# Kernel tuning notes

Hardware: AMD Instinct MI355X
Metric: run time of the kernel (lower is better)

The kernel has to match this reference:

```python
import jax, jax.numpy as jnp
import numpy as np
import math


def _alibi_slopes(h):
    # h must be a power of 2 here (h=16); matches pow2slopes in the source
    start = 2.0 ** (-2.0 ** (-(math.log2(h) - 3.0)))
    return jnp.asarray([start ** (i + 1) for i in range(h)], dtype=jnp.float32)


def setup_inputs() -> dict:
    key = jax.random.key(0)
    ks = jax.random.split(key, 7)
    B, N, d, h, r = 2, 2048, 1024, 16, 32
    dk = d // h
    x = jax.random.normal(ks[0], (B, N, d), dtype=jnp.float32)
    # causal additive mask (standard usage of the optional `mask` arg)
    i = jnp.arange(N)[:, None]
    j = jnp.arange(N)[None, :]
    mask = jnp.where(j > i, jnp.float32(-1e9), jnp.float32(0.0))[None, None]  # [1,1,N,N]
    s = 1.0 / math.sqrt(d)
    Wq = jax.random.normal(ks[1], (d, d), dtype=jnp.float32) * s
    Wk = jax.random.normal(ks[2], (d, d), dtype=jnp.float32) * s
    Wv = jax.random.normal(ks[3], (d, d), dtype=jnp.float32) * s
    # orthogonal init of U, as in nn.init.orthogonal_
    U, _ = jnp.linalg.qr(jax.random.normal(ks[4], (dk, r), dtype=jnp.float32))
    Wproj = jax.random.normal(ks[5], (d, h * r), dtype=jnp.float32) * (1.0 / math.sqrt(h * r))
    return {"x": x, "mask": mask, "Wq": Wq, "Wk": Wk, "Wv": Wv, "U": U,
            "Wproj": Wproj, "rel_bias_tokens": N}


def reference(x, mask, Wq, Wk, Wv, U, Wproj, rel_bias_tokens):
    B, N, d = x.shape
    dk, r = U.shape
    h = d // dk

    def lowrank_proj(W):
        # Linear(d,d,bias=False) then per-head low-rank projection by U
        y = (x @ W.T).reshape(B, N, h, dk)          # [B,N,h,dk]
        return jnp.einsum('bnhk,kr->bhnr', y, U)     # [B,h,N,r]

    q = lowrank_proj(Wq)
    k = lowrank_proj(Wk)
    v = lowrank_proj(Wv)

    # scores scaled by sqrt(dk) (NOT sqrt(r)) -- faithful to source
    att = jnp.einsum('bhnr,bhmr->bhnm', q, k) / math.sqrt(dk)  # [B,h,N,N]

    # q_len == k_len branch: alibi bias + mask
    i = jnp.arange(rel_bias_tokens)[:, None]
    j = jnp.arange(rel_bias_tokens)[None, :]
    dist = jnp.maximum(j - i, 0).astype(att.dtype)             # clamp_min(0)
    slopes = _alibi_slopes(h)
    att = att + (-slopes[:, None, None] * dist)[None] + mask

    z = jnp.einsum('bhnm,bhmr->bhnr', jax.nn.softmax(att, axis=-1), v)
    z = z.transpose(0, 2, 1, 3).reshape(B, N, h * r)
    # dropout is identity in eval
    return z @ Wproj.T
```

## Files before the change

kernel.cpp:

```cpp
#include <hip/hip_runtime.h>
#include <hip/hip_bf16.h>
#include <stdint.h>

typedef unsigned short u16;
typedef __attribute__((ext_vector_type(4))) short short4v;
typedef __attribute__((ext_vector_type(8))) short short8;
typedef __attribute__((ext_vector_type(4))) float f32x4;

#define NB 2
#define NN 2048
#define ND 1024
#define NH 16
#define NR 32
#define NM (NB*NN)
#define NHR 512
#define NQKV 1536

static __device__ __forceinline__ u16 f2bf(float f) {
  union { float f; uint32_t u; } v; v.f = f;
  uint32_t r = v.u + 0x7fffu + ((v.u >> 16) & 1u);
  return (u16)(r >> 16);
}
static __device__ __forceinline__ u16 fastbf(float f) {
  union { float f; uint32_t u; } v; v.f = f;
  return (u16)((v.u + 0x8000u) >> 16);
}

typedef __attribute__((address_space(1))) unsigned int as1_u32;
typedef __attribute__((address_space(3))) unsigned int as3_u32;

static __device__ __forceinline__ void async_copy16(void* lds, const void* g) {
  __builtin_amdgcn_global_load_lds((as1_u32*)(uintptr_t)g,
                                   (as3_u32*)(uint32_t)(uintptr_t)lds,
                                   16, 0, 0);
}

__global__ __launch_bounds__(256, 2)
void prep(const float* __restrict__ x, const float* __restrict__ Wproj,
          const float* __restrict__ Wq, const float* __restrict__ Wk,
          const float* __restrict__ Wv, const float* __restrict__ U,
          u16* __restrict__ xb, u16* __restrict__ Wpb, u16* __restrict__ WcT) {
  __shared__ float sU[64 * 32];
  const int blk = blockIdx.x;
  const int tid = threadIdx.x;
  if (blk < 2304) {
    const float* in = (blk < 2048) ? x : Wproj;
    u16* o = (blk < 2048) ? xb : Wpb;
    const int i = ((blk < 2048) ? blk : (blk - 2048)) * 256 + tid;
    const float4* p = (const float4*)in + (size_t)i * 2;
    float4 a = p[0], b2 = p[1];
    short8 v;
    v[0] = f2bf(a.x);  v[1] = f2bf(a.y);  v[2] = f2bf(a.z);  v[3] = f2bf(a.w);
    v[4] = f2bf(b2.x); v[5] = f2bf(b2.y); v[6] = f2bf(b2.z); v[7] = f2bf(b2.w);
    *((short8*)o + i) = v;
  } else {
    #pragma unroll
    for (int t = 0; t < 2; ++t)
      ((float4*)sU)[t * 256 + tid] = ((const float4*)U)[t * 256 + tid];
    __syncthreads();
    const int local = blk - 2304;
    const int wh = local >> 2;
    const int w = wh >> 4, head = wh & 15;
    const float* W = (w == 0) ? Wq : (w == 1 ? Wk : Wv);
    const int i = (local & 3) * 256 + tid;
    const float* Wcol = W + (size_t)head * 64 * ND + i;
    float acc[32];
    #pragma unroll
    for (int rr = 0; rr < 32; ++rr) acc[rr] = 0.f;
    for (int kk = 0; kk < 64; ++kk) {
      const float wv = Wcol[(size_t)kk * ND];
      const float4* u4 = (const float4*)&sU[kk * 32];
      #pragma unroll
      for (int r4 = 0; r4 < 8; ++r4) {
        float4 u = u4[r4];
        acc[r4 * 4 + 0] += wv * u.x;
        acc[r4 * 4 + 1] += wv * u.y;
        acc[r4 * 4 + 2] += wv * u.z;
        acc[r4 * 4 + 3] += wv * u.w;
      }
    }
    const float sc = (w == 0) ? 0.125f : 1.0f;
    const int colBase = w * 512 + head * 32;
    #pragma unroll
    for (int rr = 0; rr < 32; ++rr)
      WcT[(size_t)(colBase + rr) * ND + i] = f2bf(acc[rr] * sc);
  }
}

template<int EPI>
__global__ __launch_bounds__(256, 3)
void gemm_bt(const u16* __restrict__ A, int lda,
             const u16* __restrict__ BT, int ldb, int K,
             u16* __restrict__ o0, u16* __restrict__ o1, u16* __restrict__ o2,
             float* __restrict__ fo) {
  __shared__ __align__(16) u16 lA[64 * 64];
  __shared__ __align__(16) u16 lB[128 * 64];
  const int tid = threadIdx.x;
  const int lane = tid & 63, quad = lane >> 4, l16 = lane & 15;
  const int wave = tid >> 6;
  const int wn = wave * 32;
  const int GX = gridDim.x;
  const int flat = blockIdx.y * GX + blockIdx.x;
  const int xcd = flat & 7, s = flat >> 3;
  const int per = gridDim.y >> 3;
  const int brow = xcd * per + s / GX, bcol = s % GX;
  const int rowBase = brow * 64, colBase = bcol * 128;

  f32x4 acc[4][2];
  #pragma unroll
  for (int i = 0; i < 4; ++i)
    #pragma unroll
    for (int j = 0; j < 2; ++j)
      acc[i][j] = (f32x4){0.f, 0.f, 0.f, 0.f};

  for (int kt = 0; kt < K; kt += 64) {
    #pragma unroll
    for (int it = 0; it < 6; ++it) {
      const int cid = it * 256 + tid;
      if (it < 2) {
        const int row = cid >> 3, pc = cid & 7;
        const int gc = pc ^ (row & 7);
        async_copy16(&lA[cid * 8], &A[(size_t)(rowBase + row) * lda + kt + gc * 8]);
      } else {
        const int c2 = cid - 512;
        const int row = c2 >> 3, pc = c2 & 7;
        const int gc = pc ^ (row & 7);
        async_copy16(&lB[c2 * 8], &BT[(size_t)(colBase + row) * ldb + kt + gc * 8]);
      }
    }
    __syncthreads();
    #pragma unroll
    for (int ks = 0; ks < 64; ks += 32) {
      short8 fa[4], fb[2];
      #pragma unroll
      for (int t = 0; t < 4; ++t) {
        const int ra = t * 16 + l16;
        const int pa = ((ks >> 3) + quad) ^ (ra & 7);
        fa[t] = *(const short8*)&lA[ra * 64 + pa * 8];
      }
      #pragma unroll
      for (int t = 0; t < 2; ++t) {
        const int rb = wn + t * 16 + l16;
        const int pb = ((ks >> 3) + quad) ^ (rb & 7);
        fb[t] = *(const short8*)&lB[rb * 64 + pb * 8];
      }
      #pragma unroll
      for (int mt = 0; mt < 4; ++mt)
        #pragma unroll
        for (int nt = 0; nt < 2; ++nt)
          acc[mt][nt] = __builtin_amdgcn_mfma_f32_16x16x32_bf16(
              fa[mt], fb[nt], acc[mt][nt], 0, 0, 0);
    }
    __syncthreads();
  }

  #pragma unroll
  for (int mt = 0; mt < 4; ++mt) {
    const int gr0 = rowBase + mt * 16 + quad * 4;
    #pragma unroll
    for (int nt = 0; nt < 2; ++nt) {
      const int c = colBase + wn + nt * 16 + l16;
      #pragma unroll
      for (int j = 0; j < 4; ++j) {
        const float v = acc[mt][nt][j];
        const int row = gr0 + j;
        if (EPI == 0) {
          fo[(size_t)row * 1024 + c] = v;
        } else {
          const int b = row >> 11, n = row & (NN - 1);
          const int w = c >> 9, ch = c & 511, head = ch >> 5, rr = ch & 31;
          if (w == 0)
            o0[(size_t)(((b * NH + head) * NN + n)) * NR + rr] = f2bf(v);
          else if (w == 1)
            o1[(size_t)(((b * NH + head) * NN + n)) * NR + rr] = f2bf(v);
          else
            o2[(size_t)((b * NH + head) * NR + rr) * NN + n] = f2bf(v);
        }
      }
    }
  }
}

__global__ __launch_bounds__(256, 6)
void flash_attn(const u16* __restrict__ q, const u16* __restrict__ k,
                const u16* __restrict__ vt, u16* __restrict__ z) {
  __shared__ __align__(16) u16 lK[2][64 * 32];
  __shared__ __align__(16) u16 lV[2][32 * 64];
  const int bh = blockIdx.x;
  const int b = bh >> 4, head = bh & 15;
  const int tid = threadIdx.x;
  const int lane = tid & 63, quad = lane >> 4, l16 = lane & 15;
  const int wave = tid >> 6;
  const int qblk = gridDim.y - 1 - blockIdx.y;
  const int qb0 = qblk * 64;
  const int qbase = qb0 + wave * 16;
  const int qq = qbase + l16;

  const u16* qp = q  + (size_t)bh * NN * NR;
  const u16* kp = k  + (size_t)bh * NN * NR;
  const u16* vp = vt + (size_t)bh * NR * NN;

  const short8 bq = *(const short8*)&qp[(size_t)(qbase + l16) * NR + quad * 8];

  f32x4 Ot0 = (f32x4){0.f,0.f,0.f,0.f};
  f32x4 Ot1 = (f32x4){0.f,0.f,0.f,0.f};
  float ls = 0.f;

  const int krow = tid >> 2, kc = tid & 3;
  const int vrow = tid >> 3, vpc = tid & 7;
  const int vgc = vpc ^ (vrow & 7);

  #define STAGE(kt_, buf_) do {                                            \
    const int m0_ = (kt_) * 64;                                            \
    async_copy16(&lK[buf_][tid * 8], &kp[(size_t)(m0_ + krow) * NR + kc * 8]); \
    async_copy16(&lV[buf_][tid * 8], &vp[(size_t)vrow * NN + m0_ + vgc * 8]);  \
  } while (0)

  STAGE(0, 0);
  int buf = 0;
  for (int kt = 0; kt <= qblk; ++kt) {
    asm volatile("s_waitcnt vmcnt(0) lgkmcnt(0)" ::: "memory");
    __syncthreads();
    if (kt < qblk) STAGE(kt + 1, buf ^ 1);

    const int m0 = kt * 64;
    f32x4 s[4];
    const f32x4 zero = (f32x4){0.f,0.f,0.f,0.f};
    #pragma unroll
    for (int g = 0; g < 4; ++g) {
      const short8 ak = *(const short8*)&lK[buf][(16 * g + l16) * 32 + quad * 8];
      s[g] = __builtin_amdgcn_mfma_f32_16x16x32_bf16(ak, bq, zero, 0, 0, 0);
    }
    if (kt == qblk) {
      #pragma unroll
      for (int g = 0; g < 4; ++g)
        #pragma unroll
        for (int j = 0; j < 4; ++j)
          if (m0 + 16 * g + quad * 4 + j > qq) s[g][j] = -1e30f;
    }
    #pragma unroll
    for (int g = 0; g < 4; ++g) {
      const float p0 = __expf(s[g][0]), p1 = __expf(s[g][1]);
      const float p2 = __expf(s[g][2]), p3 = __expf(s[g][3]);
      ls += (p0 + p1) + (p2 + p3);
      short4v bp;
      bp[0] = fastbf(p0); bp[1] = fastbf(p1); bp[2] = fastbf(p2); bp[3] = fastbf(p3);
      const int c0 = 2 * g + (quad >> 1), off = (quad & 1) * 4;
      const short4v av0 = *(const short4v*)
          &lV[buf][l16 * 64 + ((c0 ^ (l16 & 7)) * 8) + off];
      const short4v av1 = *(const short4v*)
          &lV[buf][(16 + l16) * 64 + ((c0 ^ ((16 + l16) & 7)) * 8) + off];
      Ot0 = __builtin_amdgcn_mfma_f32_16x16x16bf16_1k(av0, bp, Ot0, 0, 0, 0);
      Ot1 = __builtin_amdgcn_mfma_f32_16x16x16bf16_1k(av1, bp, Ot1, 0, 0, 0);
    }
    asm volatile("s_waitcnt lgkmcnt(0)" ::: "memory");
    __syncthreads();
    buf ^= 1;
  }
  #undef STAGE

  ls += __shfl_xor(ls, 16);
  ls += __shfl_xor(ls, 32);
  const float inv = 1.f / ls;

  short4v o0, o1;
  #pragma unroll
  for (int j = 0; j < 4; ++j) {
    o0[j] = f2bf(Ot0[j] * inv);
    o1[j] = f2bf(Ot1[j] * inv);
  }
  u16* zr = z + (size_t)(b * NN + qq) * NHR + head * NR;
  *(short4v*)&zr[quad * 4]      = o0;
  *(short4v*)&zr[16 + quad * 4] = o1;
}

extern "C" void kernel_launch(void* const* d_in, const int* in_sizes, int n_in,
                              void* d_out, int out_size, void* d_ws, size_t ws_size,
                              hipStream_t stream) {
  const float* x     = (const float*)d_in[0];
  const float* Wq    = (const float*)d_in[2];
  const float* Wk    = (const float*)d_in[3];
  const float* Wv    = (const float*)d_in[4];
  const float* U     = (const float*)d_in[5];
  const float* Wproj = (const float*)d_in[6];
  float* out = (float*)d_out;

  u16* ws  = (u16*)d_ws;
  u16* xb  = ws;
  u16* z   = ws;
  u16* Wpb = ws + (size_t)4 * 1024 * 1024;
  u16* WcT = Wpb + (size_t)512 * 1024;
  u16* q   = ws + (size_t)6 * 1024 * 1024;
  u16* kk  = q  + (size_t)NB * NH * NN * NR;
  u16* vt  = kk + (size_t)NB * NH * NN * NR;

  prep<<<2496, 256, 0, stream>>>(x, Wproj, Wq, Wk, Wv, U, xb, Wpb, WcT);
  gemm_bt<1><<<dim3(NQKV / 128, NM / 64), 256, 0, stream>>>(
      xb, ND, WcT, ND, ND, q, kk, vt, nullptr);
  flash_attn<<<dim3(NB * NH, NN / 64), 256, 0, stream>>>(q, kk, vt, z);
  gemm_bt<0><<<dim3(ND / 128, NM / 64), 256, 0, stream>>>(
      z, NHR, Wpb, NHR, NHR, nullptr, nullptr, nullptr, out);
}
```

Measured before the change: 159.8 us.

## Double-buffer GEMM LDS tiles and drop the trailing attention-loop barrier

The bf16 GEMM kernel now keeps two LDS buffers for the A and B tiles. It issues the async global-to-LDS copy for the next k-tile right after the barrier, so the load overlaps the MFMA work on the current tile. The attention loop drops its end-of-iteration wait and barrier, because the top-of-loop barrier already keeps the buffer swap safe. In exchange, the GEMM's LDS footprint doubles to about 48KB per block, which may limit occupancy under the 3-blocks-per-CU launch bound.

```diff
diff --git a/kernel.cpp b/kernel.cpp
--- a/kernel.cpp
+++ b/kernel.cpp
@@ -34,6 +34,11 @@
                                    (as3_u32*)(uint32_t)(uintptr_t)lds,
                                    16, 0, 0);
 }
+
+#define SB_BARRIER() do {                                        \
+    asm volatile("s_waitcnt vmcnt(0) lgkmcnt(0)" ::: "memory");  \
+    __syncthreads();                                             \
+  } while (0)
 
 __global__ __launch_bounds__(256, 2)
 void prep(const float* __restrict__ x, const float* __restrict__ Wproj,
@@ -93,8 +98,8 @@
              const u16* __restrict__ BT, int ldb, int K,
              u16* __restrict__ o0, u16* __restrict__ o1, u16* __restrict__ o2,
              float* __restrict__ fo) {
-  __shared__ __align__(16) u16 lA[64 * 64];
-  __shared__ __align__(16) u16 lB[128 * 64];
+  __shared__ __align__(16) u16 lA[2][64 * 64];
+  __shared__ __align__(16) u16 lB[2][128 * 64];
   const int tid = threadIdx.x;
   const int lane = tid & 63, quad = lane >> 4, l16 = lane & 15;
   const int wave = tid >> 6;
@@ -113,36 +118,46 @@
     for (int j = 0; j < 2; ++j)
       acc[i][j] = (f32x4){0.f, 0.f, 0.f, 0.f};
 
-  for (int kt = 0; kt < K; kt += 64) {
-    #pragma unroll
-    for (int it = 0; it < 6; ++it) {
-      const int cid = it * 256 + tid;
-      if (it < 2) {
-        const int row = cid >> 3, pc = cid & 7;
-        const int gc = pc ^ (row & 7);
-        async_copy16(&lA[cid * 8], &A[(size_t)(rowBase + row) * lda + kt + gc * 8]);
-      } else {
-        const int c2 = cid - 512;
-        const int row = c2 >> 3, pc = c2 & 7;
-        const int gc = pc ^ (row & 7);
-        async_copy16(&lB[c2 * 8], &BT[(size_t)(colBase + row) * ldb + kt + gc * 8]);
-      }
-    }
-    __syncthreads();
+  #define GSTAGE(t_, bf_) do {                                              \
+    const int kt0 = (t_) * 64;                                              \
+    _Pragma("unroll")                                                       \
+    for (int it = 0; it < 6; ++it) {                                        \
+      const int cid = it * 256 + tid;                                       \
+      if (it < 2) {                                                         \
+        const int row = cid >> 3, pc = cid & 7;                             \
+        const int gc = pc ^ (row & 7);                                      \
+        async_copy16(&lA[bf_][cid * 8],                                     \
+                     &A[(size_t)(rowBase + row) * lda + kt0 + gc * 8]);     \
+      } else {                                                              \
+        const int c2 = cid - 512;                                           \
+        const int row = c2 >> 3, pc = c2 & 7;                               \
+        const int gc = pc ^ (row & 7);                                      \
+        async_copy16(&lB[bf_][c2 * 8],                                      \
+                     &BT[(size_t)(colBase + row) * ldb + kt0 + gc * 8]);    \
+      }                                                                     \
+    }                                                                       \
+  } while (0)
+
+  const int NT = K / 64;
+  GSTAGE(0, 0);
+  int buf = 0;
+  for (int t = 0; t < NT; ++t) {
+    SB_BARRIER();
+    if (t + 1 < NT) GSTAGE(t + 1, buf ^ 1);
     #pragma unroll
     for (int ks = 0; ks < 64; ks += 32) {
       short8 fa[4], fb[2];
       #pragma unroll
-      for (int t = 0; t < 4; ++t) {
-        const int ra = t * 16 + l16;
+      for (int t2 = 0; t2 < 4; ++t2) {
+        const int ra = t2 * 16 + l16;
         const int pa = ((ks >> 3) + quad) ^ (ra & 7);
-        fa[t] = *(const short8*)&lA[ra * 64 + pa * 8];
+        fa[t2] = *(const short8*)&lA[buf][ra * 64 + pa * 8];
       }
       #pragma unroll
-      for (int t = 0; t < 2; ++t) {
-        const int rb = wn + t * 16 + l16;
+      for (int t2 = 0; t2 < 2; ++t2) {
+        const int rb = wn + t2 * 16 + l16;
         const int pb = ((ks >> 3) + quad) ^ (rb & 7);
-        fb[t] = *(const short8*)&lB[rb * 64 + pb * 8];
+        fb[t2] = *(const short8*)&lB[buf][rb * 64 + pb * 8];
       }
       #pragma unroll
       for (int mt = 0; mt < 4; ++mt)
@@ -151,8 +166,9 @@
           acc[mt][nt] = __builtin_amdgcn_mfma_f32_16x16x32_bf16(
               fa[mt], fb[nt], acc[mt][nt], 0, 0, 0);
     }
-    __syncthreads();
-  }
+    buf ^= 1;
+  }
+  #undef GSTAGE
 
   #pragma unroll
   for (int mt = 0; mt < 4; ++mt) {
@@ -219,8 +235,7 @@
   STAGE(0, 0);
   int buf = 0;
   for (int kt = 0; kt <= qblk; ++kt) {
-    asm volatile("s_waitcnt vmcnt(0) lgkmcnt(0)" ::: "memory");
-    __syncthreads();
+    SB_BARRIER();
     if (kt < qblk) STAGE(kt + 1, buf ^ 1);
 
     const int m0 = kt * 64;
@@ -253,8 +268,6 @@
       Ot0 = __builtin_amdgcn_mfma_f32_16x16x16bf16_1k(av0, bp, Ot0, 0, 0, 0);
       Ot1 = __builtin_amdgcn_mfma_f32_16x16x16bf16_1k(av1, bp, Ot1, 0, 0, 0);
     }
-    asm volatile("s_waitcnt lgkmcnt(0)" ::: "memory");
-    __syncthreads();
     buf ^= 1;
   }
   #undef STAGE
```

After: 158.1 us. About the same (-1.1%).
